# Kernel tuning notes

Hardware: AMD Instinct MI355X
Metric: run time of the kernel (lower is better)

## Reference

```python
import jax, jax.numpy as jnp
import numpy as np
from jax import lax

E, H, D = 1024, 16, 64          # embed_dim, num_heads, head_dim
B, T = 8, 64                    # batch, decode chunk
KV = 4096                       # kv_seq_len -> cache capacity 2*KV
START = 4096                    # start_pos (prefill already filled cache[:START])
THETA = 10000.0


def setup_inputs() -> dict:
    key = jax.random.key(0)
    kx, kck, kcv, kq, kk, kv, ko = jax.random.split(key, 7)
    s = 0.02
    return {
        "x": jax.random.normal(kx, (B, T, E), jnp.float32),
        "cache_keys": jax.random.normal(kck, (B, 2 * KV, H, D), jnp.float32),
        "cache_values": jax.random.normal(kcv, (B, 2 * KV, H, D), jnp.float32),
        "Wq": jax.random.normal(kq, (E, E), jnp.float32) * s,
        "Wk": jax.random.normal(kk, (E, E), jnp.float32) * s,
        "Wv": jax.random.normal(kv, (E, E), jnp.float32) * s,
        "Wo": jax.random.normal(ko, (E, E), jnp.float32) * s,
        "start_pos": START,
    }


def _rope_bug_faithful(x, start_pos):
    # x: (B, T, H, Dd). The source helper unpacks (B,H,T,D)=x.shape on a (B,T,H,D)
    # tensor, so rotation angles are indexed by HEAD index (positions
    # start_pos..start_pos+H-1) and broadcast over the time axis. Reproduced exactly.
    Bn, Tn, Hn, Dd = x.shape
    dh = Dd // 2
    inv_freq = 1.0 / (THETA ** (jnp.arange(dh, dtype=jnp.float32) / dh))
    pos = jnp.arange(Hn, dtype=jnp.float32) + jnp.float32(start_pos)  # (H,)
    ang = pos[:, None] * inv_freq[None, :]                            # (H, dh)
    cos = jnp.cos(ang)[None, None]                                    # (1,1,H,dh)
    sin = jnp.sin(ang)[None, None]
    xr = x.reshape(Bn, Tn, Hn, dh, 2)
    x0, x1 = xr[..., 0], xr[..., 1]
    o0 = x0 * cos - x1 * sin
    o1 = x0 * sin + x1 * cos
    return jnp.stack([o0, o1], axis=-1).reshape(Bn, Tn, Hn, Dd)


def reference(x, cache_keys, cache_values, Wq, Wk, Wv, Wo, start_pos):
    Bn, Tn, C = x.shape
    Hn, Dd = cache_keys.shape[2], cache_keys.shape[3]
    scale = 1.0 / np.sqrt(Dd).astype(np.float32)
    end = start_pos + Tn

    q = (x @ Wq).reshape(Bn, Tn, Hn, Dd)
    k = (x @ Wk).reshape(Bn, Tn, Hn, Dd)
    v = (x @ Wv).reshape(Bn, Tn, Hn, Dd)

    q = _rope_bug_faithful(q, start_pos)
    k = _rope_bug_faithful(k, start_pos)

    # cache append at dynamic offset (detached in source)
    ck = lax.dynamic_update_slice_in_dim(cache_keys, lax.stop_gradient(k), start_pos, axis=1)
    cv = lax.dynamic_update_slice_in_dim(cache_values, lax.stop_gradient(v), start_pos, axis=1)
    k_full = lax.stop_gradient(ck[:, :end])  # (B, S, H, D), S = end
    v_full = lax.stop_gradient(cv[:, :end])

    qh = q.transpose(0, 2, 1, 3)        # (B,H,T,D)
    kh = k_full.transpose(0, 2, 1, 3)   # (B,H,S,D)
    vh = v_full.transpose(0, 2, 1, 3)

    scores = jnp.einsum("bhtd,bhsd->bhts", qh, kh) * scale  # (B,H,T,S)
    i = jnp.arange(Tn)[:, None]
    j = jnp.arange(end)[None, :]
    allowed = j <= (start_pos + i)      # intended causal mask over cache span
    neg = jnp.finfo(scores.dtype).min
    scores = jnp.where(allowed[None, None], scores, neg)
    attn = jax.nn.softmax(scores, axis=-1)
    ctx = jnp.einsum("bhts,bhsd->bhtd", attn, vh)
    out = ctx.transpose(0, 2, 1, 3).reshape(Bn, Tn, C) @ Wo
    return out
```

## Files before the change

### kernel.cpp

```cpp
#include <hip/hip_runtime.h>
#include <hip/hip_bf16.h>
#include <math.h>

typedef __attribute__((ext_vector_type(8))) __bf16 bf16x8;
typedef __attribute__((ext_vector_type(4))) __bf16 bf16x4;
typedef __attribute__((ext_vector_type(4))) float f32x4;

#define EE 1024
#define HH 16
#define DD 64
#define BB 8
#define TT 64
#define NSPLIT 8

__device__ __forceinline__ f32x4 mfma16(bf16x8 a, bf16x8 b, f32x4 c) {
    return __builtin_amdgcn_mfma_f32_16x16x32_bf16(a, b, c, 0, 0, 0);
}

__global__ __launch_bounds__(256) void k_qkv(const float* __restrict__ x, const float* __restrict__ Wq,
                                             const float* __restrict__ Wk, const float* __restrict__ Wv,
                                             const int* __restrict__ sp_ptr,
                                             __bf16* __restrict__ qws, __bf16* __restrict__ knew,
                                             __bf16* __restrict__ vnew) {
    __shared__ __bf16 a_lds[64][72];
    __shared__ __bf16 b_lds[64][68];
    __shared__ float cs_l[32], sn_l[32];
    int xcd = blockIdx.x & 7, idx = blockIdx.x >> 3;
    int bn = xcd * 6 + idx % 6;
    int bm = idx / 6;
    int wsel = bn >> 4;
    int n0 = (bn & 15) * 64;
    int m0 = bm * 64;
    const float* W = (wsel == 0) ? Wq : (wsel == 1) ? Wk : Wv;
    int tid = threadIdx.x;
    int wv = tid >> 6, lane = tid & 63;
    int l16 = lane & 15, lhi = lane >> 4;
    int g = tid >> 4, m4 = (tid & 15) * 4;

    f32x4 acc[4];
#pragma unroll
    for (int f = 0; f < 4; ++f) acc[f] = (f32x4){0.f, 0.f, 0.f, 0.f};

    f32x4 areg[4], breg[4];
#pragma unroll
    for (int p = 0; p < 4; ++p)
        areg[p] = *(const f32x4*)&x[(size_t)(m0 + p * 16 + g) * EE + m4];
#pragma unroll
    for (int i = 0; i < 4; ++i)
        breg[i] = *(const f32x4*)&W[(size_t)(4 * g + i) * EE + n0 + m4];

    if (tid < 32) {
        int h = bn & 15;
        int sp = sp_ptr[0];
        float invf = powf(10000.0f, -(float)tid / 32.0f);
        float ang = (float)(sp + h) * invf;
        float s, c;
        sincosf(ang, &s, &c);
        cs_l[tid] = c;
        sn_l[tid] = s;
    }

    for (int kt = 0; kt < 16; ++kt) {
        __syncthreads();
#pragma unroll
        for (int p = 0; p < 4; ++p) {
            bf16x4 a4 = { (__bf16)areg[p][0], (__bf16)areg[p][1], (__bf16)areg[p][2], (__bf16)areg[p][3] };
            *(bf16x4*)&a_lds[p * 16 + g][m4] = a4;
        }
#pragma unroll
        for (int j = 0; j < 4; ++j) {
            bf16x4 t4 = { (__bf16)breg[0][j], (__bf16)breg[1][j], (__bf16)breg[2][j], (__bf16)breg[3][j] };
            *(bf16x4*)&b_lds[m4 + j][4 * g] = t4;
        }
        if (kt < 15) {
            int ko = (kt + 1) * 64;
#pragma unroll
            for (int p = 0; p < 4; ++p)
                areg[p] = *(const f32x4*)&x[(size_t)(m0 + p * 16 + g) * EE + ko + m4];
#pragma unroll
            for (int i = 0; i < 4; ++i)
                breg[i] = *(const f32x4*)&W[(size_t)(ko + 4 * g + i) * EE + n0 + m4];
        }
        __syncthreads();
        bf16x8 a0 = *(bf16x8*)&a_lds[wv * 16 + l16][lhi * 8];
        bf16x8 a1 = *(bf16x8*)&a_lds[wv * 16 + l16][32 + lhi * 8];
#pragma unroll
        for (int f = 0; f < 4; ++f) {
            bf16x8 b0 = *(bf16x8*)&b_lds[f * 16 + l16][lhi * 8];
            bf16x8 b1 = *(bf16x8*)&b_lds[f * 16 + l16][32 + lhi * 8];
            acc[f] = mfma16(a0, b0, acc[f]);
            acc[f] = mfma16(a1, b1, acc[f]);
        }
    }
    __bf16* dst = (wsel == 0) ? qws : (wsel == 1) ? knew : vnew;
    int h = bn & 15;
#pragma unroll
    for (int f = 0; f < 4; ++f) {
#pragma unroll
        for (int r = 0; r < 4; ++r) {
            float v = acc[f][r];
            int row = m0 + wv * 16 + lhi * 4 + r;
            int d = f * 16 + l16;
            float o = v;
            if (wsel < 2) {
                float other = __shfl_xor(v, 1);
                int pp = d >> 1;
                float c = cs_l[pp], s = sn_l[pp];
                o = ((d & 1) == 0) ? (v * c - other * s) : (other * s + v * c);
            }
            int b = row >> 6, t = row & 63;
            dst[((size_t)((b * HH + h) * TT + t)) * DD + d] = (__bf16)o;
        }
    }
}

__global__ __launch_bounds__(256, 4) void k_attn(const __bf16* __restrict__ qws, const __bf16* __restrict__ knew,
                                                 const __bf16* __restrict__ vnew,
                                                 const float* __restrict__ ck, const float* __restrict__ cv,
                                                 __bf16* __restrict__ Opart, float2* __restrict__ mlpart) {
    __shared__ __bf16 k_lds[64][72];
    __shared__ __bf16 vT_lds[64][68];
    __shared__ __bf16 p_lds[64][72];
    int bh = blockIdx.x >> 3, split = blockIdx.x & 7;
    int b = bh >> 4, h = bh & 15;
    int tid = threadIdx.x, wv = tid >> 6, lane = tid & 63;
    int l16 = lane & 15, lhi = lane >> 4;
    int g = tid >> 4, m4 = (tid & 15) * 4;

    bf16x8 qf0, qf1;
    {
        const __bf16* qp = qws + ((size_t)bh * TT + (wv * 16 + l16)) * DD;
        qf0 = *(const bf16x8*)&qp[lhi * 8];
        qf1 = *(const bf16x8*)&qp[32 + lhi * 8];
    }
    f32x4 acc[4];
#pragma unroll
    for (int f = 0; f < 4; ++f) acc[f] = (f32x4){0.f, 0.f, 0.f, 0.f};
    float m[4], l[4];
#pragma unroll
    for (int r = 0; r < 4; ++r) { m[r] = -1e30f; l[r] = 0.f; }

    const float* ckb = ck + (size_t)b * 8192 * EE + h * DD;
    const float* cvb = cv + (size_t)b * 8192 * EE + h * DD;
    int s0 = split * 512;

    auto compute = [&](bool mask) {
        f32x4 sf[4];
#pragma unroll
        for (int f = 0; f < 4; ++f) {
            f32x4 z = (f32x4){0.f, 0.f, 0.f, 0.f};
            bf16x8 b0 = *(bf16x8*)&k_lds[f * 16 + l16][lhi * 8];
            bf16x8 b1 = *(bf16x8*)&k_lds[f * 16 + l16][32 + lhi * 8];
            z = mfma16(qf0, b0, z);
            z = mfma16(qf1, b1, z);
            sf[f] = z;
        }
#pragma unroll
        for (int f = 0; f < 4; ++f) {
#pragma unroll
            for (int r = 0; r < 4; ++r) {
                float sv = sf[f][r] * 0.125f;
                if (mask) {
                    int t_row = wv * 16 + lhi * 4 + r;
                    int s_loc = f * 16 + l16;
                    if (s_loc > t_row) sv = -1e30f;
                }
                sf[f][r] = sv;
            }
        }
        float mt[4];
#pragma unroll
        for (int r = 0; r < 4; ++r)
            mt[r] = fmaxf(fmaxf(sf[0][r], sf[1][r]), fmaxf(sf[2][r], sf[3][r]));
#pragma unroll
        for (int off = 1; off < 16; off <<= 1) {
#pragma unroll
            for (int r = 0; r < 4; ++r) mt[r] = fmaxf(mt[r], __shfl_xor(mt[r], off));
        }
        float fac[4];
#pragma unroll
        for (int r = 0; r < 4; ++r) {
            float mn = fmaxf(m[r], mt[r]);
            fac[r] = __expf(m[r] - mn);
            m[r] = mn;
        }
        float ladd[4] = {0.f, 0.f, 0.f, 0.f};
#pragma unroll
        for (int f = 0; f < 4; ++f) {
#pragma unroll
            for (int r = 0; r < 4; ++r) {
                float pv = __expf(sf[f][r] - m[r]);
                sf[f][r] = pv;
                ladd[r] += pv;
            }
        }
#pragma unroll
        for (int off = 1; off < 16; off <<= 1) {
#pragma unroll
            for (int r = 0; r < 4; ++r) ladd[r] += __shfl_xor(ladd[r], off);
        }
#pragma unroll
        for (int r = 0; r < 4; ++r) l[r] = l[r] * fac[r] + ladd[r];
#pragma unroll
        for (int f = 0; f < 4; ++f)
#pragma unroll
            for (int r = 0; r < 4; ++r) acc[f][r] *= fac[r];
#pragma unroll
        for (int f = 0; f < 4; ++f)
#pragma unroll
            for (int r = 0; r < 4; ++r)
                p_lds[wv * 16 + lhi * 4 + r][f * 16 + l16] = (__bf16)sf[f][r];
        bf16x8 pa0 = *(bf16x8*)&p_lds[wv * 16 + l16][lhi * 8];
        bf16x8 pa1 = *(bf16x8*)&p_lds[wv * 16 + l16][32 + lhi * 8];
#pragma unroll
        for (int f = 0; f < 4; ++f) {
            bf16x8 v0 = *(bf16x8*)&vT_lds[f * 16 + l16][lhi * 8];
            bf16x8 v1 = *(bf16x8*)&vT_lds[f * 16 + l16][32 + lhi * 8];
            acc[f] = mfma16(pa0, v0, acc[f]);
            acc[f] = mfma16(pa1, v1, acc[f]);
        }
    };

    f32x4 kreg[4], vreg[4];
#pragma unroll
    for (int p = 0; p < 4; ++p)
        kreg[p] = *(const f32x4*)&ckb[(size_t)(s0 + p * 16 + g) * EE + m4];
#pragma unroll
    for (int i = 0; i < 4; ++i)
        vreg[i] = *(const f32x4*)&cvb[(size_t)(s0 + 4 * g + i) * EE + m4];

    for (int it = 0; it < 8; ++it) {
#pragma unroll
        for (int p = 0; p < 4; ++p) {
            bf16x4 k4 = { (__bf16)kreg[p][0], (__bf16)kreg[p][1], (__bf16)kreg[p][2], (__bf16)kreg[p][3] };
            *(bf16x4*)&k_lds[p * 16 + g][m4] = k4;
        }
#pragma unroll
        for (int j = 0; j < 4; ++j) {
            bf16x4 tv = { (__bf16)vreg[0][j], (__bf16)vreg[1][j], (__bf16)vreg[2][j], (__bf16)vreg[3][j] };
            *(bf16x4*)&vT_lds[m4 + j][4 * g] = tv;
        }
        if (it < 7) {
            int sb = s0 + (it + 1) * 64;
#pragma unroll
            for (int p = 0; p < 4; ++p)
                kreg[p] = *(const f32x4*)&ckb[(size_t)(sb + p * 16 + g) * EE + m4];
#pragma unroll
            for (int i = 0; i < 4; ++i)
                vreg[i] = *(const f32x4*)&cvb[(size_t)(sb + 4 * g + i) * EE + m4];
        }
        __syncthreads();
        compute(false);
        __syncthreads();
    }

    if (split == 7) {
#pragma unroll
        for (int p = 0; p < 2; ++p) {
            int idx = p * 256 + tid;
            int r = idx >> 3, c8 = (idx & 7) * 8;
            *(bf16x8*)&k_lds[r][c8] = *(const bf16x8*)&knew[((size_t)bh * TT + r) * DD + c8];
            bf16x8 vf = *(const bf16x8*)&vnew[((size_t)bh * TT + r) * DD + c8];
#pragma unroll
            for (int j = 0; j < 8; ++j) vT_lds[c8 + j][r] = vf[j];
        }
        __syncthreads();
        compute(true);
    }

#pragma unroll
    for (int f = 0; f < 4; ++f)
#pragma unroll
        for (int r = 0; r < 4; ++r) {
            int t = wv * 16 + lhi * 4 + r;
            int d = f * 16 + l16;
            Opart[(((size_t)split * 128 + bh) * TT + t) * DD + d] = (__bf16)acc[f][r];
        }
    if (l16 == 0) {
#pragma unroll
        for (int r = 0; r < 4; ++r) {
            int t = wv * 16 + lhi * 4 + r;
            mlpart[((size_t)split * 128 + bh) * TT + t] = make_float2(m[r], l[r]);
        }
    }
}

__global__ __launch_bounds__(256) void k_combine(const __bf16* __restrict__ Opart, const float2* __restrict__ mlpart,
                                                 __bf16* __restrict__ ctxb) {
    int idx = blockIdx.x * 256 + threadIdx.x;
    int d = idx & 63, t = (idx >> 6) & 63, bh = idx >> 12;
    float ms[NSPLIT], ls[NSPLIT];
    float mg = -1e30f;
#pragma unroll
    for (int s = 0; s < NSPLIT; ++s) {
        float2 ml = mlpart[((size_t)s * 128 + bh) * TT + t];
        ms[s] = ml.x; ls[s] = ml.y;
        mg = fmaxf(mg, ms[s]);
    }
    float den = 0.f, num = 0.f;
#pragma unroll
    for (int s = 0; s < NSPLIT; ++s) {
        float w = __expf(ms[s] - mg);
        den += ls[s] * w;
        num += (float)Opart[(((size_t)s * 128 + bh) * TT + t) * DD + d] * w;
    }
    float ctx = num / den;
    int b = bh >> 4, hh = bh & 15;
    ctxb[(size_t)(b * TT + t) * EE + hh * DD + d] = (__bf16)ctx;
}

__global__ __launch_bounds__(256) void k_oproj(const __bf16* __restrict__ ctxb, const float* __restrict__ Wo,
                                               float* __restrict__ out) {
    __shared__ __bf16 a_lds[64][72];
    __shared__ __bf16 b_lds[64][68];
    int xcd = blockIdx.x & 7, idx = blockIdx.x >> 3;
    int bn = xcd * 2 + (idx & 1);
    int bm = idx >> 1;
    int n0 = bn * 64, m0 = bm * 64;
    int tid = threadIdx.x;
    int wv = tid >> 6, lane = tid & 63;
    int l16 = lane & 15, lhi = lane >> 4;
    int g = tid >> 4, m4 = (tid & 15) * 4;
    int r0 = tid >> 3, c8 = (tid & 7) * 8;
    f32x4 acc[4];
#pragma unroll
    for (int f = 0; f < 4; ++f) acc[f] = (f32x4){0.f, 0.f, 0.f, 0.f};

    bf16x8 ar0 = *(const bf16x8*)&ctxb[(size_t)(m0 + r0) * EE + c8];
    bf16x8 ar1 = *(const bf16x8*)&ctxb[(size_t)(m0 + 32 + r0) * EE + c8];
    f32x4 breg[4];
#pragma unroll
    for (int i = 0; i < 4; ++i)
        breg[i] = *(const f32x4*)&Wo[(size_t)(4 * g + i) * EE + n0 + m4];

    for (int kt = 0; kt < 16; ++kt) {
        __syncthreads();
        *(bf16x8*)&a_lds[r0][c8] = ar0;
        *(bf16x8*)&a_lds[32 + r0][c8] = ar1;
#pragma unroll
        for (int j = 0; j < 4; ++j) {
            bf16x4 t4 = { (__bf16)breg[0][j], (__bf16)breg[1][j], (__bf16)breg[2][j], (__bf16)breg[3][j] };
            *(bf16x4*)&b_lds[m4 + j][4 * g] = t4;
        }
        if (kt < 15) {
            int ko = (kt + 1) * 64;
            ar0 = *(const bf16x8*)&ctxb[(size_t)(m0 + r0) * EE + ko + c8];
            ar1 = *(const bf16x8*)&ctxb[(size_t)(m0 + 32 + r0) * EE + ko + c8];
#pragma unroll
            for (int i = 0; i < 4; ++i)
                breg[i] = *(const f32x4*)&Wo[(size_t)(ko + 4 * g + i) * EE + n0 + m4];
        }
        __syncthreads();
        bf16x8 a0 = *(bf16x8*)&a_lds[wv * 16 + l16][lhi * 8];
        bf16x8 a1 = *(bf16x8*)&a_lds[wv * 16 + l16][32 + lhi * 8];
#pragma unroll
        for (int f = 0; f < 4; ++f) {
            bf16x8 b0 = *(bf16x8*)&b_lds[f * 16 + l16][lhi * 8];
            bf16x8 b1 = *(bf16x8*)&b_lds[f * 16 + l16][32 + lhi * 8];
            acc[f] = mfma16(a0, b0, acc[f]);
            acc[f] = mfma16(a1, b1, acc[f]);
        }
    }
#pragma unroll
    for (int f = 0; f < 4; ++f)
#pragma unroll
        for (int r = 0; r < 4; ++r) {
            int row = m0 + wv * 16 + lhi * 4 + r;
            out[(size_t)row * EE + n0 + f * 16 + l16] = acc[f][r];
        }
}

extern "C" void kernel_launch(void* const* d_in, const int* in_sizes, int n_in,
                              void* d_out, int out_size, void* d_ws, size_t ws_size,
                              hipStream_t stream) {
    const float* x  = (const float*)d_in[0];
    const float* ck = (const float*)d_in[1];
    const float* cv = (const float*)d_in[2];
    const float* Wq = (const float*)d_in[3];
    const float* Wk = (const float*)d_in[4];
    const float* Wv = (const float*)d_in[5];
    const float* Wo = (const float*)d_in[6];
    const int* sp   = (const int*)d_in[7];
    float* out = (float*)d_out;

    char* p = (char*)d_ws;
    __bf16* qws = (__bf16*)p;           p += (size_t)524288 * 2;
    __bf16* knew = (__bf16*)p;          p += (size_t)524288 * 2;
    __bf16* vnew = (__bf16*)p;          p += (size_t)524288 * 2;
    __bf16* Opart = (__bf16*)p;         p += (size_t)NSPLIT * 128 * 64 * 64 * 2;
    float2* mlpart = (float2*)p;        p += (size_t)NSPLIT * 8192 * 8;
    __bf16* ctxb = (__bf16*)p;          p += (size_t)524288 * 2;

    k_qkv<<<384, 256, 0, stream>>>(x, Wq, Wk, Wv, sp, qws, knew, vnew);
    k_attn<<<BB * HH * NSPLIT, 256, 0, stream>>>(qws, knew, vnew, ck, cv, Opart, mlpart);
    k_combine<<<2048, 256, 0, stream>>>(Opart, mlpart, ctxb);
    k_oproj<<<128, 256, 0, stream>>>(ctxb, Wo, out);
}
```

Baseline: 88.45 us.

## Fuse split-KV combine into attention kernel via last-block atomic counter

Removes the separate combine kernel launch. Each attention block now increments a per-(batch,head) atomic counter after writing its partial output, and the last split to finish performs the log-sum-exp merge with vectorized bf16 loads and stores. Counters are zeroed inside the QKV kernel. The split index is also moved to the high bits of the block index, which changes the scheduling order across XCDs. In exchange it adds threadfences and an atomic per block, and the combine work is serialized onto one block per head.

New measurement: 260.5 us. +194.5%, slower.

```diff
diff --git a/kernel.cpp b/kernel.cpp
--- a/kernel.cpp
+++ b/kernel.cpp
@@ -21,10 +21,12 @@
                                              const float* __restrict__ Wk, const float* __restrict__ Wv,
                                              const int* __restrict__ sp_ptr,
                                              __bf16* __restrict__ qws, __bf16* __restrict__ knew,
-                                             __bf16* __restrict__ vnew) {
+                                             __bf16* __restrict__ vnew, int* __restrict__ counter) {
     __shared__ __bf16 a_lds[64][72];
     __shared__ __bf16 b_lds[64][68];
     __shared__ float cs_l[32], sn_l[32];
+    int tid = threadIdx.x;
+    if (blockIdx.x == 0 && tid < 128) counter[tid] = 0;
     int xcd = blockIdx.x & 7, idx = blockIdx.x >> 3;
     int bn = xcd * 6 + idx % 6;
     int bm = idx / 6;
@@ -32,7 +34,6 @@
     int n0 = (bn & 15) * 64;
     int m0 = bm * 64;
     const float* W = (wsel == 0) ? Wq : (wsel == 1) ? Wk : Wv;
-    int tid = threadIdx.x;
     int wv = tid >> 6, lane = tid & 63;
     int l16 = lane & 15, lhi = lane >> 4;
     int g = tid >> 4, m4 = (tid & 15) * 4;
@@ -117,11 +118,13 @@
 __global__ __launch_bounds__(256, 4) void k_attn(const __bf16* __restrict__ qws, const __bf16* __restrict__ knew,
                                                  const __bf16* __restrict__ vnew,
                                                  const float* __restrict__ ck, const float* __restrict__ cv,
-                                                 __bf16* __restrict__ Opart, float2* __restrict__ mlpart) {
+                                                 __bf16* __restrict__ Opart, float2* __restrict__ mlpart,
+                                                 int* __restrict__ counter, __bf16* __restrict__ ctxb) {
     __shared__ __bf16 k_lds[64][72];
     __shared__ __bf16 vT_lds[64][68];
     __shared__ __bf16 p_lds[64][72];
-    int bh = blockIdx.x >> 3, split = blockIdx.x & 7;
+    __shared__ int last_flag;
+    int split = blockIdx.x >> 7, bh = blockIdx.x & 127;
     int b = bh >> 4, h = bh & 15;
     int tid = threadIdx.x, wv = tid >> 6, lane = tid & 63;
     int l16 = lane & 15, lhi = lane >> 4;
@@ -283,12 +286,18 @@
             mlpart[((size_t)split * 128 + bh) * TT + t] = make_float2(m[r], l[r]);
         }
     }
-}
-
-__global__ __launch_bounds__(256) void k_combine(const __bf16* __restrict__ Opart, const float2* __restrict__ mlpart,
-                                                 __bf16* __restrict__ ctxb) {
-    int idx = blockIdx.x * 256 + threadIdx.x;
-    int d = idx & 63, t = (idx >> 6) & 63, bh = idx >> 12;
+
+    __threadfence();
+    if (tid == 0) {
+        int prev = atomicAdd(&counter[bh], 1);
+        last_flag = (prev == NSPLIT - 1);
+    }
+    __syncthreads();
+    if (!last_flag) return;
+    __threadfence();
+
+    int t = tid >> 2;
+    int d0 = (tid & 3) * 16;
     float ms[NSPLIT], ls[NSPLIT];
     float mg = -1e30f;
 #pragma unroll
@@ -297,16 +306,26 @@
         ms[s] = ml.x; ls[s] = ml.y;
         mg = fmaxf(mg, ms[s]);
     }
-    float den = 0.f, num = 0.f;
+    float den = 0.f, num[16];
+#pragma unroll
+    for (int j = 0; j < 16; ++j) num[j] = 0.f;
 #pragma unroll
     for (int s = 0; s < NSPLIT; ++s) {
         float w = __expf(ms[s] - mg);
         den += ls[s] * w;
-        num += (float)Opart[(((size_t)s * 128 + bh) * TT + t) * DD + d] * w;
-    }
-    float ctx = num / den;
-    int b = bh >> 4, hh = bh & 15;
-    ctxb[(size_t)(b * TT + t) * EE + hh * DD + d] = (__bf16)ctx;
+        const __bf16* op = &Opart[(((size_t)s * 128 + bh) * TT + t) * DD + d0];
+        bf16x8 o0 = *(const bf16x8*)&op[0];
+        bf16x8 o1 = *(const bf16x8*)&op[8];
+#pragma unroll
+        for (int j = 0; j < 8; ++j) { num[j] += (float)o0[j] * w; num[8 + j] += (float)o1[j] * w; }
+    }
+    float inv = 1.0f / den;
+    bf16x8 c0, c1;
+#pragma unroll
+    for (int j = 0; j < 8; ++j) { c0[j] = (__bf16)(num[j] * inv); c1[j] = (__bf16)(num[8 + j] * inv); }
+    __bf16* cp = &ctxb[(size_t)(b * TT + t) * EE + h * DD + d0];
+    *(bf16x8*)&cp[0] = c0;
+    *(bf16x8*)&cp[8] = c1;
 }
 
 __global__ __launch_bounds__(256) void k_oproj(const __bf16* __restrict__ ctxb, const float* __restrict__ Wo,
@@ -390,9 +409,9 @@
     __bf16* Opart = (__bf16*)p;         p += (size_t)NSPLIT * 128 * 64 * 64 * 2;
     float2* mlpart = (float2*)p;        p += (size_t)NSPLIT * 8192 * 8;
     __bf16* ctxb = (__bf16*)p;          p += (size_t)524288 * 2;
-
-    k_qkv<<<384, 256, 0, stream>>>(x, Wq, Wk, Wv, sp, qws, knew, vnew);
-    k_attn<<<BB * HH * NSPLIT, 256, 0, stream>>>(qws, knew, vnew, ck, cv, Opart, mlpart);
-    k_combine<<<2048, 256, 0, stream>>>(Opart, mlpart, ctxb);
+    int* counter = (int*)p;             p += 512;
+
+    k_qkv<<<384, 256, 0, stream>>>(x, Wq, Wk, Wv, sp, qws, knew, vnew, counter);
+    k_attn<<<BB * HH * NSPLIT, 256, 0, stream>>>(qws, knew, vnew, ck, cv, Opart, mlpart, counter, ctxb);
     k_oproj<<<128, 256, 0, stream>>>(ctxb, Wo, out);
 }
```
